# Kernel tuning notes

Hardware: AMD Instinct MI355X
Metric: run time of the kernel (lower is better)

Reference implementation:

```python
import math
import jax, jax.numpy as jnp
import numpy as np

D_MODEL = 4096
N_Q_HEADS = 32
N_KV_HEADS = 8
HEAD_DIM = D_MODEL // N_Q_HEADS  # 128
N_GROUPS = N_Q_HEADS // N_KV_HEADS  # 4
B, S = 1, 2048


def setup_inputs() -> dict:
    key = jax.random.key(0)
    k1, k2, k3, k4, k5 = jax.random.split(key, 5)
    scale = 1.0 / math.sqrt(D_MODEL)
    return {
        "x": jax.random.normal(k1, (B, S, D_MODEL), dtype=jnp.float32),
        "W_q": jax.random.normal(k2, (N_Q_HEADS * HEAD_DIM, D_MODEL), dtype=jnp.float32) * scale,
        "W_k": jax.random.normal(k3, (N_KV_HEADS * HEAD_DIM, D_MODEL), dtype=jnp.float32) * scale,
        "W_v": jax.random.normal(k4, (N_KV_HEADS * HEAD_DIM, D_MODEL), dtype=jnp.float32) * scale,
        "W_o": jax.random.normal(k5, (D_MODEL, D_MODEL), dtype=jnp.float32) * scale,
    }


def reference(x, W_q, W_k, W_v, W_o):
    Bsz, Sq, _ = x.shape
    # projections (nn.Linear, no bias): y = x @ W.T
    q = (x @ W_q.T).reshape(Bsz, Sq, N_Q_HEADS, HEAD_DIM).transpose(0, 2, 1, 3)   # [B,Hq,S,d]
    k = (x @ W_k.T).reshape(Bsz, Sq, N_KV_HEADS, HEAD_DIM).transpose(0, 2, 1, 3)  # [B,Hkv,S,d]
    v = (x @ W_v.T).reshape(Bsz, Sq, N_KV_HEADS, HEAD_DIM).transpose(0, 2, 1, 3)
    # physical KV head repeat (repeat_interleave over head dim)
    k_rep = jnp.repeat(k, N_GROUPS, axis=1)  # [B,Hq,S,d]
    v_rep = jnp.repeat(v, N_GROUPS, axis=1)
    scores = jnp.einsum("bhqd,bhkd->bhqk", q, k_rep) / math.sqrt(HEAD_DIM)
    attn = jax.nn.softmax(scores, axis=-1)  # no causal mask in the original
    out = jnp.einsum("bhqk,bhkd->bhqd", attn, v_rep)
    out = out.transpose(0, 2, 1, 3).reshape(Bsz, Sq, D_MODEL)
    out = out @ W_o.T
    # original returns first n_kv_heads slices of the REPEATED k/v as the "cache"
    return out, (k_rep[:, :N_KV_HEADS], v_rep[:, :N_KV_HEADS])
```

## Files before the change

kernel.cpp:

```cpp
#include <hip/hip_runtime.h>
#include <hip/hip_bf16.h>

typedef __bf16 bf16;
typedef float f32x4 __attribute__((ext_vector_type(4)));
typedef float f32x16 __attribute__((ext_vector_type(16)));
typedef bf16 bf16x8 __attribute__((ext_vector_type(8)));
typedef bf16 bf16x2 __attribute__((ext_vector_type(2)));
typedef unsigned u32x4 __attribute__((ext_vector_type(4)));

#define MFMA16(a,b,c) __builtin_amdgcn_mfma_f32_16x16x32_bf16((a),(b),(c),0,0,0)
#define MFMA32(a,b,c) __builtin_amdgcn_mfma_f32_32x32x16_bf16((a),(b),(c),0,0,0)

__device__ __forceinline__ void gload16(const void* g, void* l) {
    __builtin_amdgcn_global_load_lds((const __attribute__((address_space(1))) unsigned*)g,
                                     (__attribute__((address_space(3))) unsigned*)l, 16, 0, 0);
}

__device__ __forceinline__ unsigned pk(float lo, float hi) {
    bf16x2 t; t[0] = (bf16)lo; t[1] = (bf16)hi;
    return __builtin_bit_cast(unsigned, t);
}

__device__ __forceinline__ void cvt8(const float* __restrict__ in, bf16* __restrict__ out, int i) {
    const float4* p = (const float4*)in + (size_t)i * 2;
    float4 a = p[0], b = p[1];
    bf16x8 o;
    o[0]=(bf16)a.x; o[1]=(bf16)a.y; o[2]=(bf16)a.z; o[3]=(bf16)a.w;
    o[4]=(bf16)b.x; o[5]=(bf16)b.y; o[6]=(bf16)b.z; o[7]=(bf16)b.w;
    *((bf16x8*)out + i) = o;
}

__global__ __launch_bounds__(256) void cvt_all(const float* __restrict__ x, const float* __restrict__ wq,
                                               const float* __restrict__ wk, const float* __restrict__ wv,
                                               bf16* __restrict__ xb, bf16* __restrict__ wqkv) {
    int i = blockIdx.x * 256 + threadIdx.x;
    const float* src; bf16* dst; int n8;
    switch (blockIdx.y) {
        case 0: src = x;  dst = xb;                 n8 = 1048576; break;
        case 1: src = wq; dst = wqkv;               n8 = 2097152; break;
        case 2: src = wk; dst = wqkv + 16777216;    n8 = 524288;  break;
        default: src = wv; dst = wqkv + 20971520;   n8 = 524288;  break;
    }
    if (i < n8) cvt8(src, dst, i);
}

__global__ __launch_bounds__(256) void cvt_one(const float* __restrict__ in, bf16* __restrict__ out, int n8) {
    int i = blockIdx.x * 256 + threadIdx.x;
    if (i < n8) cvt8(in, out, i);
}

__device__ __forceinline__ void stage_tile(const bf16* __restrict__ A, const bf16* __restrict__ B,
                                           int K, int bm, int bn, int k0,
                                           bf16* As, bf16* Bs, int wv, int lane) {
#pragma unroll
    for (int i=0;i<4;++i) {
        int off = i*4096 + wv*1024 + lane*16;
        int row = off >> 7;
        int cg = (lane & 7) ^ (row & 7);
        gload16(A + (size_t)(bm+row)*K + k0 + cg*8, (char*)As + i*4096 + wv*1024);
    }
#pragma unroll
    for (int i=0;i<4;++i) {
        int off = i*4096 + wv*1024 + lane*16;
        int row = off >> 7;
        int cg = (lane & 7) ^ (row & 7);
        gload16(B + (size_t)(bn+row)*K + k0 + cg*8, (char*)Bs + i*4096 + wv*1024);
    }
}

__device__ __forceinline__ void gemm_core(const bf16* __restrict__ A, const bf16* __restrict__ B,
                                          int K, int bm, int bn, bf16* As, bf16* Bs, f32x4 (&acc)[4][4]) {
    const int tid = threadIdx.x, lane = tid & 63, wv = tid >> 6;
    const int wr = wv >> 1, wc = wv & 1, lr = lane & 15, ls = lane >> 4;

#pragma unroll
    for (int mm=0;mm<4;++mm)
#pragma unroll
        for (int nn=0;nn<4;++nn)
#pragma unroll
            for (int r=0;r<4;++r) acc[mm][nn][r] = 0.f;

    stage_tile(A, B, K, bm, bn, 0, As, Bs, wv, lane);
    __syncthreads();

    for (int k0 = 0; k0 < K; k0 += 64) {
        const int cur = (k0 >> 6) & 1;
        bf16* AsC = As + cur * 8192;
        bf16* BsC = Bs + cur * 8192;
        if (k0 + 64 < K)
            stage_tile(A, B, K, bm, bn, k0 + 64, As + (cur^1)*8192, Bs + (cur^1)*8192, wv, lane);

#pragma unroll
        for (int ks=0; ks<2; ++ks) {
            bf16x8 af[4], bfr[4];
#pragma unroll
            for (int mm=0;mm<4;++mm) {
                int row = wr*64 + mm*16 + lr;
                af[mm] = *(const bf16x8*)((char*)AsC + row*128 + (((ks*4+ls) ^ (row&7))<<4));
            }
#pragma unroll
            for (int nn=0;nn<4;++nn) {
                int row = wc*64 + nn*16 + lr;
                bfr[nn] = *(const bf16x8*)((char*)BsC + row*128 + (((ks*4+ls) ^ (row&7))<<4));
            }
#pragma unroll
            for (int mm=0;mm<4;++mm)
#pragma unroll
                for (int nn=0;nn<4;++nn) acc[mm][nn] = MFMA16(af[mm], bfr[nn], acc[mm][nn]);
        }
        __syncthreads();
    }
}

__global__ __launch_bounds__(256) void gemm_qkv(const bf16* __restrict__ A, const bf16* __restrict__ W,
                                                bf16* __restrict__ C, float qscale) {
    __shared__ __align__(16) bf16 As[2*128*64];
    __shared__ __align__(16) bf16 Bs[2*128*64];
    int flat = blockIdx.y * gridDim.x + blockIdx.x;
    int id = (flat & 7) * 96 + (flat >> 3);
    int bm = (id & 15) * 128, bn = (id >> 4) * 128;
    f32x4 acc[4][4];
    gemm_core(A, W, 4096, bm, bn, As, Bs, acc);

    const float s = (bn < 4096) ? qscale : 1.0f;
    const int lane = threadIdx.x & 63, wv = threadIdx.x >> 6;
    const int wr = wv >> 1, wc = wv & 1, lr = lane & 15, ls = lane >> 4;
#pragma unroll
    for (int mm=0;mm<4;++mm)
#pragma unroll
        for (int nn=0;nn<4;++nn)
#pragma unroll
            for (int r=0;r<4;++r) {
                int mg = bm + wr*64 + mm*16 + ls*4 + r;
                int ng = bn + wc*64 + nn*16 + lr;
                C[(size_t)mg * 6144 + ng] = (bf16)(acc[mm][nn][r] * s);
            }
}

__global__ __launch_bounds__(256) void gemm_o(const bf16* __restrict__ A, const bf16* __restrict__ B,
                                              float* __restrict__ Cp) {
    __shared__ __align__(16) bf16 As[2*128*64];
    __shared__ __align__(16) bf16 Bs[2*128*64];
    int flat = blockIdx.y * gridDim.x + blockIdx.x;
    int id = (flat & 7) * 64 + (flat >> 3);
    int bm = (id & 15) * 128, bn = (id >> 4) * 128;
    f32x4 acc[4][4];
    gemm_core(A, B, 4096, bm, bn, As, Bs, acc);

    const int lane = threadIdx.x & 63, wv = threadIdx.x >> 6;
    const int wr = wv >> 1, wc = wv & 1, lr = lane & 15, ls = lane >> 4;
#pragma unroll
    for (int mm=0;mm<4;++mm)
#pragma unroll
        for (int nn=0;nn<4;++nn)
#pragma unroll
            for (int r=0;r<4;++r) {
                int mg = bm + wr*64 + mm*16 + ls*4 + r;
                int ng = bn + wc*64 + nn*16 + lr;
                Cp[(size_t)mg * 4096 + ng] = acc[mm][nn][r];
            }
}

__global__ __launch_bounds__(256) void trans_cache(const bf16* __restrict__ QKVb, bf16* __restrict__ Vt,
                                                   float* __restrict__ cacheK, float* __restrict__ cacheV) {
    int b = blockIdx.x;
    if (b < 512) {
        __shared__ bf16 t[64][70];
        int dt = b & 15, st = b >> 4;
        int tt = threadIdx.x;
        int r = tt >> 2, c0 = (tt & 3) * 16;
#pragma unroll
        for (int i = 0; i < 2; ++i) {
            bf16x8 v = *(const bf16x8*)(QKVb + (size_t)(st*64 + r)*6144 + 5120 + dt*64 + c0 + i*8);
#pragma unroll
            for (int j = 0; j < 8; ++j) t[c0 + i*8 + j][r] = v[j];
        }
        __syncthreads();
        int c = tt >> 2, r0 = (tt & 3) * 16;
#pragma unroll
        for (int i = 0; i < 2; ++i) {
            bf16x8 v = *(const bf16x8*)(&t[c][r0 + i*8]);
            *(bf16x8*)(Vt + (size_t)(dt*64 + c)*2048 + st*64 + r0 + i*8) = v;
        }
    } else {
        int g = (b - 512) * 256 + threadIdx.x;
        int d8 = g & 15, s = (g >> 4) & 2047, j = (g >> 15) & 7, kv = g >> 18;
        int hk = j >> 2;
        bf16x8 v = *(const bf16x8*)(QKVb + (size_t)s*6144 + 4096 + kv*1024 + hk*128 + d8*8);
        float* dst = (kv ? cacheV : cacheK) + ((size_t)j*2048 + s)*128 + d8*8;
        float4 lo, hi;
        lo.x=(float)v[0]; lo.y=(float)v[1]; lo.z=(float)v[2]; lo.w=(float)v[3];
        hi.x=(float)v[4]; hi.y=(float)v[5]; hi.z=(float)v[6]; hi.w=(float)v[7];
        *(float4*)dst = lo;
        *(float4*)(dst + 4) = hi;
    }
}

__device__ __forceinline__ void stage_kv(const bf16* __restrict__ QKVb, const bf16* __restrict__ Vt,
                                         char* Ks, char* Vs, int kvh, int kt, int buf,
                                         int wv, int lane) {
#pragma unroll
    for (int i=0;i<2;++i) {
        int off = i*8192 + wv*1024 + lane*16;
        int row = off >> 8;
        int cg = (lane & 15) ^ (row & 7);
        gload16(QKVb + (size_t)(kt*64+row)*6144 + 4096 + kvh*128 + cg*8, Ks + buf*16384 + i*8192 + wv*1024);
    }
#pragma unroll
    for (int i=0;i<2;++i) {
        int off = i*8192 + wv*1024 + lane*16;
        int d = off >> 7;
        int cg = (lane & 7) ^ (d & 7);
        gload16(Vt + (size_t)(kvh*128+d)*2048 + kt*64 + cg*8, Vs + buf*16384 + i*8192 + wv*1024);
    }
}

__global__ __launch_bounds__(512) void flash_attn(const bf16* __restrict__ QKVb, const bf16* __restrict__ Vt,
                                                  bf16* __restrict__ AO) {
    __shared__ __align__(16) char Ks[2*16384];
    __shared__ __align__(16) char Vs[2*16384];
    const int tid = threadIdx.x, lane = tid & 63, wq = tid >> 6;
    const int l31 = lane & 31, hi = lane >> 5;
    const int h = blockIdx.y, kvh = h >> 2;
    const int q0w = blockIdx.x * 256 + wq * 32;

    bf16x8 qf[8];
#pragma unroll
    for (int f=0; f<8; ++f)
        qf[f] = *(const bf16x8*)(QKVb + (size_t)(q0w + l31)*6144 + h*128 + f*16 + hi*8);

    f32x16 acc[4];
#pragma unroll
    for (int db=0;db<4;++db)
#pragma unroll
        for (int r=0;r<16;++r) acc[db][r] = 0.f;
    float mrun = -1e30f, lrun = 0.f;

    stage_kv(QKVb, Vt, Ks, Vs, kvh, 0, 0, wq, lane);
    __syncthreads();

    for (int t = 0; t < 32; ++t) {
        const int cur = t & 1;
        if (t + 1 < 32) stage_kv(QKVb, Vt, Ks, Vs, kvh, t+1, cur^1, wq, lane);

        const char* KsB = Ks + cur*16384;
        f32x16 sc[2];
#pragma unroll
        for (int kc=0;kc<2;++kc)
#pragma unroll
            for (int r=0;r<16;++r) sc[kc][r] = 0.f;
#pragma unroll
        for (int f=0; f<8; ++f) {
            int r0 = l31, r1 = 32 + l31;
            bf16x8 k0 = *(const bf16x8*)(KsB + r0*256 + (((f*2+hi) ^ (r0&7))<<4));
            bf16x8 k1 = *(const bf16x8*)(KsB + r1*256 + (((f*2+hi) ^ (r1&7))<<4));
            sc[0] = MFMA32(k0, qf[f], sc[0]);
            sc[1] = MFMA32(k1, qf[f], sc[1]);
        }

        float tmax = sc[0][0];
#pragma unroll
        for (int r=1;r<16;++r) tmax = fmaxf(tmax, sc[0][r]);
#pragma unroll
        for (int r=0;r<16;++r) tmax = fmaxf(tmax, sc[1][r]);
        tmax = fmaxf(tmax, __shfl_xor(tmax, 32, 64));
        if (!__all(tmax <= mrun + 8.f)) {
            float mnew = fmaxf(mrun, tmax);
            float corr = __expf(mrun - mnew);
            mrun = mnew;
            lrun *= corr;
#pragma unroll
            for (int r=0;r<16;++r) {
                float cr = __shfl(corr, (r&3) + 8*(r>>2) + 4*hi, 64);
#pragma unroll
                for (int db=0;db<4;++db) acc[db][r] *= cr;
            }
        }
        float rs = 0.f;
#pragma unroll
        for (int kc=0;kc<2;++kc)
#pragma unroll
            for (int r=0;r<16;++r) { float e = __expf(sc[kc][r] - mrun); sc[kc][r] = e; rs += e; }
        rs += __shfl_xor(rs, 32, 64);
        lrun += rs;

        bf16x8 pa[4];
#pragma unroll
        for (int kb=0;kb<4;++kb) {
            const int kc = kb>>1, r0 = (kb&1)*8;
            unsigned a0 = pk(sc[kc][r0+0], sc[kc][r0+1]);
            unsigned a1 = pk(sc[kc][r0+2], sc[kc][r0+3]);
            unsigned b0 = pk(sc[kc][r0+4], sc[kc][r0+5]);
            unsigned b1 = pk(sc[kc][r0+6], sc[kc][r0+7]);
            unsigned sa0 = (unsigned)__shfl_xor((int)a0, 32, 64);
            unsigned sa1 = (unsigned)__shfl_xor((int)a1, 32, 64);
            unsigned sb0 = (unsigned)__shfl_xor((int)b0, 32, 64);
            unsigned sb1 = (unsigned)__shfl_xor((int)b1, 32, 64);
            u32x4 w;
            w[0] = hi ? sb0 : a0;
            w[1] = hi ? sb1 : a1;
            w[2] = hi ? b0 : sa0;
            w[3] = hi ? b1 : sa1;
            pa[kb] = __builtin_bit_cast(bf16x8, w);
        }

        const char* VsB = Vs + cur*16384;
#pragma unroll
        for (int db=0;db<4;++db) {
            const int d = db*32 + l31;
#pragma unroll
            for (int kb=0;kb<4;++kb) {
                bf16x8 vf = *(const bf16x8*)(VsB + d*128 + (((kb*2+hi) ^ (d&7))<<4));
                acc[db] = MFMA32(pa[kb], vf, acc[db]);
            }
        }
        __syncthreads();
    }

    float linv = 1.0f / lrun;
#pragma unroll
    for (int r=0;r<16;++r) {
        int crw = (r&3) + 8*(r>>2) + 4*hi;
        float lv = __shfl(linv, crw, 64);
        size_t qrow = (size_t)q0w + crw;
#pragma unroll
        for (int db=0;db<4;++db)
            AO[qrow*4096 + h*128 + db*32 + l31] = (bf16)(acc[db][r] * lv);
    }
}

extern "C" void kernel_launch(void* const* d_in, const int* in_sizes, int n_in,
                              void* d_out, int out_size, void* d_ws, size_t ws_size,
                              hipStream_t stream) {
    const float* x  = (const float*)d_in[0];
    const float* Wq = (const float*)d_in[1];
    const float* Wk = (const float*)d_in[2];
    const float* Wv = (const float*)d_in[3];
    const float* Wo = (const float*)d_in[4];

    bf16* xb   = (bf16*)d_ws;
    bf16* QKVb = xb + (size_t)8388608;
    bf16* Wqkv = QKVb + (size_t)12582912;
    bf16* Vt  = xb;
    bf16* Wob = Wqkv;
    bf16* AO  = Wqkv + (size_t)16777216;

    float* out = (float*)d_out;
    float* cacheK = out + (size_t)8388608;
    float* cacheV = cacheK + (size_t)2097152;

    const float qscale = 0.08838834764831845f;

    cvt_all<<<dim3(8192, 4), 256, 0, stream>>>(x, Wq, Wk, Wv, xb, Wqkv);
    gemm_qkv<<<dim3(16, 48), 256, 0, stream>>>(xb, Wqkv, QKVb, qscale);
    cvt_one<<<8192, 256, 0, stream>>>(Wo, Wob, 2097152);
    trans_cache<<<2560, 256, 0, stream>>>(QKVb, Vt, cacheK, cacheV);
    flash_attn<<<dim3(8, 32), 512, 0, stream>>>(QKVb, Vt, AO);
    gemm_o<<<dim3(16, 32), 256, 0, stream>>>(AO, Wob, out);
}
```

Measured before the change: 340.6 us.

## Prefetch two tiles ahead with explicit vmcnt waits and register-staged fragments

Restructures the GEMM main loop so global-to-LDS loads run two K-tiles ahead instead of one. All LDS fragments for both k-substeps are read into registers first, then a barrier frees the buffer so the next prefetch can target it while the MFMAs run. Explicit s_waitcnt vmcnt counts replace the full __syncthreads, and s_setprio raises wave priority around the MFMA block. The goal is to hide global load latency better, at the cost of more fragment registers and fragile hand-counted waitcnt values.

Result: faster. 321.6 us (-5.6%).

```diff
diff --git a/kernel.cpp b/kernel.cpp
--- a/kernel.cpp
+++ b/kernel.cpp
@@ -57,14 +57,14 @@
         int off = i*4096 + wv*1024 + lane*16;
         int row = off >> 7;
         int cg = (lane & 7) ^ (row & 7);
-        gload16(A + (size_t)(bm+row)*K + k0 + cg*8, (char*)As + i*4096 + wv*1024);
+        gload16(A + (size_t)(bm+row)*K + k0 + cg*8, (char*)As + off);
     }
 #pragma unroll
     for (int i=0;i<4;++i) {
         int off = i*4096 + wv*1024 + lane*16;
         int row = off >> 7;
         int cg = (lane & 7) ^ (row & 7);
-        gload16(B + (size_t)(bn+row)*K + k0 + cg*8, (char*)Bs + i*4096 + wv*1024);
+        gload16(B + (size_t)(bn+row)*K + k0 + cg*8, (char*)Bs + off);
     }
 }
 
@@ -80,35 +80,51 @@
 #pragma unroll
             for (int r=0;r<4;++r) acc[mm][nn][r] = 0.f;
 
-    stage_tile(A, B, K, bm, bn, 0, As, Bs, wv, lane);
-    __syncthreads();
-
-    for (int k0 = 0; k0 < K; k0 += 64) {
-        const int cur = (k0 >> 6) & 1;
+    const int nt = K >> 6;
+    stage_tile(A, B, K, bm, bn, 0,  As,        Bs,        wv, lane);
+    stage_tile(A, B, K, bm, bn, 64, As + 8192, Bs + 8192, wv, lane);
+
+    for (int t = 0; t < nt; ++t) {
+        const int cur = t & 1;
         bf16* AsC = As + cur * 8192;
         bf16* BsC = Bs + cur * 8192;
-        if (k0 + 64 < K)
-            stage_tile(A, B, K, bm, bn, k0 + 64, As + (cur^1)*8192, Bs + (cur^1)*8192, wv, lane);
-
+
+        if (t < nt - 1) asm volatile("s_waitcnt vmcnt(8)" ::: "memory");
+        else            asm volatile("s_waitcnt vmcnt(0)" ::: "memory");
+        __builtin_amdgcn_s_barrier();
+        __builtin_amdgcn_sched_barrier(0);
+
+        bf16x8 af[2][4], bfr[2][4];
 #pragma unroll
         for (int ks=0; ks<2; ++ks) {
-            bf16x8 af[4], bfr[4];
 #pragma unroll
             for (int mm=0;mm<4;++mm) {
                 int row = wr*64 + mm*16 + lr;
-                af[mm] = *(const bf16x8*)((char*)AsC + row*128 + (((ks*4+ls) ^ (row&7))<<4));
+                af[ks][mm] = *(const bf16x8*)((char*)AsC + row*128 + (((ks*4+ls) ^ (row&7))<<4));
             }
 #pragma unroll
             for (int nn=0;nn<4;++nn) {
                 int row = wc*64 + nn*16 + lr;
-                bfr[nn] = *(const bf16x8*)((char*)BsC + row*128 + (((ks*4+ls) ^ (row&7))<<4));
-            }
+                bfr[ks][nn] = *(const bf16x8*)((char*)BsC + row*128 + (((ks*4+ls) ^ (row&7))<<4));
+            }
+        }
+        asm volatile("s_waitcnt lgkmcnt(0)" ::: "memory");
+        __builtin_amdgcn_sched_barrier(0);
+        __builtin_amdgcn_s_barrier();
+        __builtin_amdgcn_sched_barrier(0);
+
+        if (t + 2 < nt)
+            stage_tile(A, B, K, bm, bn, (t+2) << 6, AsC, BsC, wv, lane);
+
+        __builtin_amdgcn_s_setprio(1);
+#pragma unroll
+        for (int ks=0; ks<2; ++ks)
 #pragma unroll
             for (int mm=0;mm<4;++mm)
 #pragma unroll
-                for (int nn=0;nn<4;++nn) acc[mm][nn] = MFMA16(af[mm], bfr[nn], acc[mm][nn]);
-        }
-        __syncthreads();
+                for (int nn=0;nn<4;++nn)
+                    acc[mm][nn] = MFMA16(af[ks][mm], bfr[ks][nn], acc[mm][nn]);
+        __builtin_amdgcn_s_setprio(0);
     }
 }
 
```
